# Performance work log

Measured on AMD Instinct MI355X. Metric: run time of the kernel, lower is better.

Reference implementation:

```python
import jax, jax.numpy as jnp
import numpy as np

HEAD_NUM = 16
KEY_DIM = 64
EMBED = 1024
KV_OUT = HEAD_NUM * KEY_DIM  # 1024


def setup_inputs() -> dict:
    key = jax.random.key(0)
    ks = jax.random.split(key, 11)
    B, L, E = 2, 2048, EMBED
    scale = 0.02
    return {
        "query": jax.random.normal(ks[0], (B, L, E), jnp.float32),
        "key": jax.random.normal(ks[1], (B, L, E), jnp.float32),
        "value": jax.random.normal(ks[2], (B, L, E), jnp.float32),
        "W_Query": jax.random.normal(ks[3], (E, KV_OUT), jnp.float32) * scale,
        "W_Key": jax.random.normal(ks[4], (E, KV_OUT), jnp.float32) * scale,
        "W_Value": jax.random.normal(ks[5], (E, KV_OUT), jnp.float32) * scale,
        "W_Output": jax.random.normal(ks[6], (KV_OUT, E), jnp.float32) * scale,
        "B_Query": jnp.zeros((KV_OUT,), jnp.float32),
        "B_Key": jnp.zeros((KV_OUT,), jnp.float32),
        "B_Value": jnp.zeros((KV_OUT,), jnp.float32),
        "B_Output": jnp.zeros((E,), jnp.float32),
    }


def reference(query, key, value, W_Query, W_Key, W_Value, W_Output,
              B_Query, B_Key, B_Value, B_Output):
    B, Lq, E = query.shape
    Lk = key.shape[1]
    H, D = HEAD_NUM, KEY_DIM
    # QKV projections + bias
    q = query @ W_Query + B_Query            # [B, Lq, H*D]
    k = key @ W_Key + B_Key                  # [B, Lk, H*D]
    v = value @ W_Value + B_Value            # [B, Lk, H*D]
    # tf.split(axis=2) per head == reshape to [B, L, H, D]
    q = q.reshape(B, Lq, H, D)
    k = k.reshape(B, Lk, H, D)
    v = v.reshape(B, Lk, H, D)
    # scaled dot-product attention (no mask, dropout=0)
    scores = jnp.einsum("bqhd,bkhd->bhqk", q, k) / (D ** 0.5)
    probs = jax.nn.softmax(scores, axis=-1)
    out = jnp.einsum("bhqk,bkhd->bqhd", probs, v)  # [B, Lq, H, D]
    out = out.reshape(B, Lq, H * D)
    return out @ W_Output + B_Output
```

## Files before the change

kernel.cpp:

```cpp
#include <hip/hip_runtime.h>

using u16 = unsigned short;
using u32 = unsigned int;

typedef __attribute__((ext_vector_type(8))) short bf16x8;
typedef __attribute__((ext_vector_type(4))) float f32x4;
typedef __attribute__((ext_vector_type(4))) u32 u32x4;
typedef __attribute__((ext_vector_type(2))) u32 u32x2;
typedef __attribute__((ext_vector_type(4))) _Float16 f16x4;

#define MFMA_BF16_K32(a, b, c) __builtin_amdgcn_mfma_f32_16x16x32_bf16((a), (b), (c), 0, 0, 0)
#define MFMA_F16_K16(a, b, c) __builtin_amdgcn_mfma_f32_16x16x16f16((a), (b), (c), 0, 0, 0)

#define QSCALE 0.18033688011112042f

extern "C" __device__ float __ocml_native_exp2_f32(float);

__device__ __forceinline__ u16 f2bf(float f) {
  u32 u = __builtin_bit_cast(u32, f);
  return (u16)((u + 0x7fffu + ((u >> 16) & 1u)) >> 16);
}

__device__ __forceinline__ u32 pk_f16(float a, float b) {
  auto v = __builtin_amdgcn_cvt_pkrtz(a, b);
  return __builtin_bit_cast(u32, v);
}

__device__ __forceinline__ void load_lds16(const void* g, void* l) {
  __builtin_amdgcn_global_load_lds((__attribute__((address_space(1))) void*)g,
                                   (__attribute__((address_space(3))) void*)l,
                                   16, 0, 0);
}

#define W0 asm volatile("s_waitcnt vmcnt(0)" ::: "memory")
#define W3 asm volatile("s_waitcnt vmcnt(3)" ::: "memory")
#define W4 asm volatile("s_waitcnt vmcnt(4)" ::: "memory")
#define W8 asm volatile("s_waitcnt vmcnt(8)" ::: "memory")
#define W12 asm volatile("s_waitcnt vmcnt(12)" ::: "memory")
#define LGKM0 asm volatile("s_waitcnt lgkmcnt(0)" ::: "memory")
#define BARRIER                      \
  do {                               \
    __builtin_amdgcn_s_barrier();    \
    asm volatile("" ::: "memory");   \
  } while (0)

__global__ __launch_bounds__(256) void cvt_all_kernel(
    const float* __restrict__ q, const float* __restrict__ k, const float* __restrict__ v,
    u16* __restrict__ oq, u16* __restrict__ ok, u16* __restrict__ ov,
    const float* __restrict__ w0, const float* __restrict__ w1,
    const float* __restrict__ w2, const float* __restrict__ w3,
    u16* __restrict__ d0, u16* __restrict__ d1,
    u16* __restrict__ d2, u16* __restrict__ d3) {
  const int id = blockIdx.x;
  const int tid = threadIdx.x;
  if (id < 6144) {
    const int z = id >> 11, bx = id & 2047;
    const float* s = z == 0 ? q : z == 1 ? k : v;
    u16* d = z == 0 ? oq : z == 1 ? ok : ov;
    int i = (bx * 256 + tid) * 8;
    f32x4 a = *(const f32x4*)(s + i);
    f32x4 b = *(const f32x4*)(s + i + 4);
    u32x4 o;
    o.x = (u32)f2bf(a.x) | ((u32)f2bf(a.y) << 16);
    o.y = (u32)f2bf(a.z) | ((u32)f2bf(a.w) << 16);
    o.z = (u32)f2bf(b.x) | ((u32)f2bf(b.y) << 16);
    o.w = (u32)f2bf(b.z) | ((u32)f2bf(b.w) << 16);
    *(u32x4*)(d + i) = o;
    return;
  }
  __shared__ float t[64][65];
  const int r0 = id - 6144;
  const int z = r0 >> 8, rr0 = r0 & 255;
  const int bx = rr0 & 15, by = rr0 >> 4;
  const float* src = z == 0 ? w0 : z == 1 ? w1 : z == 2 ? w2 : w3;
  u16* dst = z == 0 ? d0 : z == 1 ? d1 : z == 2 ? d2 : d3;
  const float scale = (z == 0) ? QSCALE : 1.0f;
  const int r = tid >> 4, c4 = (tid & 15) * 4;
#pragma unroll
  for (int i = 0; i < 4; ++i) {
    int row = r + i * 16;
    f32x4 vv = *(const f32x4*)(src + (by * 64 + row) * 1024 + bx * 64 + c4);
    t[row][c4 + 0] = vv.x;
    t[row][c4 + 1] = vv.y;
    t[row][c4 + 2] = vv.z;
    t[row][c4 + 3] = vv.w;
  }
  __syncthreads();
  const int rw = tid >> 2, cc = (tid & 3) * 16;
  alignas(16) u16 tmp[16];
#pragma unroll
  for (int j = 0; j < 16; ++j) tmp[j] = f2bf(t[cc + j][rw] * scale);
  u32x4* outp = (u32x4*)(dst + (bx * 64 + rw) * 1024 + by * 64 + cc);
  outp[0] = *(const u32x4*)&tmp[0];
  outp[1] = *(const u32x4*)&tmp[8];
}

#define QKV_STAGE(BUF, KB)                                                    \
  {                                                                           \
    _Pragma("unroll") for (int t = 0; t < 2; ++t) {                           \
      int c = (wave * 2 + t) * 64 + lane;                                     \
      int row = c >> 2, pc = c & 3, sc = pc ^ ((row >> 1) & 3);               \
      load_lds16(A + (m0 + row) * 1024 + (KB) * 32 + sc * 8,                  \
                 &As[BUF][((wave * 2 + t) * 64) * 8]);                        \
    }                                                                         \
    _Pragma("unroll") for (int t = 0; t < 2; ++t) {                           \
      int c = (wave * 2 + t) * 64 + lane;                                     \
      int row = c >> 2, pc = c & 3, sc = pc ^ ((row >> 1) & 3);               \
      load_lds16(Bt + (n0 + row) * 1024 + (KB) * 32 + sc * 8,                 \
                 &Bs[BUF][((wave * 2 + t) * 64) * 8]);                        \
    }                                                                         \
  }

__global__ __launch_bounds__(256) void gemm_qkv_kernel(
    const u16* __restrict__ x0, const u16* __restrict__ x1, const u16* __restrict__ x2,
    const u16* __restrict__ w0, const u16* __restrict__ w1, const u16* __restrict__ w2,
    const float* __restrict__ b0, const float* __restrict__ b1, const float* __restrict__ b2,
    u16* __restrict__ c0, u16* __restrict__ c1, u16* __restrict__ vt) {
  __shared__ u16 As[2][128 * 32];
  __shared__ u16 Bs[2][128 * 32];
  const int lid = blockIdx.x;
  const int xcd = lid & 7, rr = lid >> 3;
  const int nb = rr & 7, slot = rr >> 3;
  const int g = slot * 8 + xcd;
  const int z = g >> 5, m_idx = g & 31;
  const u16* A = z == 0 ? x0 : z == 1 ? x1 : x2;
  const u16* Bt = z == 0 ? w0 : z == 1 ? w1 : w2;
  const float* bias = z == 0 ? b0 : z == 1 ? b1 : b2;
  const float bscale = z == 0 ? QSCALE : 1.0f;
  const int tid = threadIdx.x;
  const int wave = tid >> 6, lane = tid & 63;
  const int l16 = lane & 15, quad = lane >> 4;
  const int wm = wave >> 1, wn = wave & 1;
  const int m0 = m_idx * 128, n0 = nb * 128;

  f32x4 acc[4][4];
  const f32x4 zf = {0.f, 0.f, 0.f, 0.f};
#pragma unroll
  for (int i = 0; i < 4; ++i)
#pragma unroll
    for (int j = 0; j < 4; ++j) acc[i][j] = zf;

  QKV_STAGE(0, 0);
  QKV_STAGE(1, 1);

  const int chq = (l16 >> 1) & 3;
  for (int kb = 0; kb < 32; ++kb) {
    const int cur = kb & 1;
    if (kb < 31) W4; else W0;
    BARRIER;
    bf16x8 af[4], bfv[4];
#pragma unroll
    for (int mt = 0; mt < 4; ++mt)
      af[mt] = *(const bf16x8*)&As[cur][(wm * 64 + mt * 16 + l16) * 32 + (quad ^ chq) * 8];
#pragma unroll
    for (int nt = 0; nt < 4; ++nt)
      bfv[nt] = *(const bf16x8*)&Bs[cur][(wn * 64 + nt * 16 + l16) * 32 + (quad ^ chq) * 8];
#pragma unroll
    for (int mt = 0; mt < 4; ++mt)
#pragma unroll
      for (int nt = 0; nt < 4; ++nt) acc[mt][nt] = MFMA_BF16_K32(af[mt], bfv[nt], acc[mt][nt]);
    LGKM0;
    BARRIER;
    if (kb + 2 < 32) QKV_STAGE(cur, kb + 2);
  }

  float bv[4];
#pragma unroll
  for (int nt = 0; nt < 4; ++nt) bv[nt] = bias[n0 + wn * 64 + nt * 16 + l16] * bscale;
  if (z != 2) {
    u16* C = z == 0 ? c0 : c1;
#pragma unroll
    for (int mt = 0; mt < 4; ++mt)
#pragma unroll
      for (int nt = 0; nt < 4; ++nt)
#pragma unroll
        for (int r = 0; r < 4; ++r) {
          int row = m0 + wm * 64 + mt * 16 + quad * 4 + r;
          int col = n0 + wn * 64 + nt * 16 + l16;
          C[row * 1024 + col] = f2bf(acc[mt][nt][r] + bv[nt]);
        }
  } else {
#pragma unroll
    for (int mt = 0; mt < 4; ++mt)
#pragma unroll
      for (int nt = 0; nt < 4; ++nt) {
        int kvb = m0 + wm * 64 + mt * 16 + quad * 4;
        int bb = kvb >> 11, kv = kvb & 2047;
        int col = n0 + wn * 64 + nt * 16 + l16;
        int h = col >> 6, dt = (col >> 4) & 3, ld = col & 15;
        int pair = bb * 16 + h;
        int kb2 = kv >> 7, chunk = (kv >> 4) & 7, qd = (kv >> 2) & 3;
        f16x4 hv;
#pragma unroll
        for (int r = 0; r < 4; ++r) hv[r] = (_Float16)(acc[mt][nt][r] + bv[nt]);
        u16* dst = vt + ((((pair * 16 + kb2) * 8 + chunk) * 4 + dt) * 256) + qd * 64 + ld * 4;
        *(f16x4*)dst = hv;
      }
  }
}

#define OUT_STAGE(BUF, KB)                                                    \
  {                                                                           \
    {                                                                         \
      int c = wave * 64 + lane;                                               \
      int row = c >> 2, pc = c & 3, sc = pc ^ ((row >> 1) & 3);               \
      load_lds16(A + (m0 + row) * 1024 + (KB) * 32 + sc * 8,                  \
                 &As[BUF][(wave * 64) * 8]);                                  \
    }                                                                         \
    _Pragma("unroll") for (int t = 0; t < 2; ++t) {                           \
      int c = (wave * 2 + t) * 64 + lane;                                     \
      int row = c >> 2, pc = c & 3, sc = pc ^ ((row >> 1) & 3);               \
      load_lds16(Bt + (n0 + row) * 1024 + (KB) * 32 + sc * 8,                 \
                 &Bs[BUF][((wave * 2 + t) * 64) * 8]);                        \
    }                                                                         \
  }

__global__ __launch_bounds__(256) void gemm_out_kernel(const u16* __restrict__ A,
                                                       const u16* __restrict__ Bt,
                                                       const float* __restrict__ bias,
                                                       float* __restrict__ C) {
  __shared__ u16 As[2][64 * 32];
  __shared__ u16 Bs[2][128 * 32];
  const int lid = blockIdx.x;
  const int xcd = lid & 7, rr = lid >> 3;
  const int nb = rr & 7, slot = rr >> 3;
  const int by = slot * 8 + xcd;
  const int tid = threadIdx.x;
  const int wave = tid >> 6, lane = tid & 63;
  const int l16 = lane & 15, quad = lane >> 4;
  const int m0 = by * 64, n0 = nb * 128;

  f32x4 acc[4][2];
  const f32x4 zf = {0.f, 0.f, 0.f, 0.f};
#pragma unroll
  for (int i = 0; i < 4; ++i)
#pragma unroll
    for (int j = 0; j < 2; ++j) acc[i][j] = zf;

  OUT_STAGE(0, 0);
  OUT_STAGE(1, 1);

  const int chq = (l16 >> 1) & 3;
  for (int kb = 0; kb < 32; ++kb) {
    const int cur = kb & 1;
    if (kb < 31) W3; else W0;
    BARRIER;
    bf16x8 af[4], bfv[2];
#pragma unroll
    for (int mt = 0; mt < 4; ++mt)
      af[mt] = *(const bf16x8*)&As[cur][(mt * 16 + l16) * 32 + (quad ^ chq) * 8];
#pragma unroll
    for (int nt = 0; nt < 2; ++nt)
      bfv[nt] = *(const bf16x8*)&Bs[cur][(wave * 32 + nt * 16 + l16) * 32 + (quad ^ chq) * 8];
#pragma unroll
    for (int mt = 0; mt < 4; ++mt)
#pragma unroll
      for (int nt = 0; nt < 2; ++nt) acc[mt][nt] = MFMA_BF16_K32(af[mt], bfv[nt], acc[mt][nt]);
    LGKM0;
    BARRIER;
    if (kb + 2 < 32) OUT_STAGE(cur, kb + 2);
  }

  float bv[2];
#pragma unroll
  for (int nt = 0; nt < 2; ++nt) bv[nt] = bias[n0 + wave * 32 + nt * 16 + l16];
#pragma unroll
  for (int mt = 0; mt < 4; ++mt)
#pragma unroll
    for (int nt = 0; nt < 2; ++nt)
#pragma unroll
      for (int r = 0; r < 4; ++r) {
        int row = m0 + mt * 16 + quad * 4 + r;
        int col = n0 + wave * 32 + nt * 16 + l16;
        C[row * 1024 + col] = acc[mt][nt][r] + bv[nt];
      }
}

union PU { u32 u[2]; f16x4 v; };

#define QK_EXP(CUR, PKV)                                                          \
  _Pragma("unroll") for (int c2 = 0; c2 < 2; ++c2) {                              \
    const int chunk = wave * 2 + c2;                                              \
    f32x4 s_acc[4];                                                               \
    _Pragma("unroll") for (int qn = 0; qn < 4; ++qn) s_acc[qn] = zf;              \
    _Pragma("unroll") for (int ks = 0; ks < 2; ++ks) {                            \
      bf16x8 kf = *(const bf16x8*)&k_lds[CUR][(chunk * 16 + l16) * 64 +           \
                                              ((ks * 4 + quad) ^ l7) * 8];        \
      _Pragma("unroll") for (int qn = 0; qn < 4; ++qn)                            \
        s_acc[qn] = MFMA_BF16_K32(kf, qf[qn][ks], s_acc[qn]);                     \
    }                                                                             \
    _Pragma("unroll") for (int qn = 0; qn < 4; ++qn) {                            \
      float e0 = __ocml_native_exp2_f32(s_acc[qn].x);                             \
      float e1 = __ocml_native_exp2_f32(s_acc[qn].y);                             \
      float e2 = __ocml_native_exp2_f32(s_acc[qn].z);                             \
      float e3 = __ocml_native_exp2_f32(s_acc[qn].w);                             \
      lp[qn] += (e0 + e1) + (e2 + e3);                                            \
      PKV[c2][qn].u[0] = pk_f16(e0, e1);                                          \
      PKV[c2][qn].u[1] = pk_f16(e2, e3);                                          \
    }                                                                             \
  }

#define FLASH_BODY(KB, CUR, VCUR, VNXT, PFV, PFK, WAIT)                           \
  {                                                                               \
    BARRIER;                                                                      \
    if (PFV) {                                                                    \
      const u16* vp = Vh + ((KB) + 1) * 8192;                                     \
      _Pragma("unroll") for (int c2 = 0; c2 < 2; ++c2)                            \
        _Pragma("unroll") for (int dt = 0; dt < 4; ++dt)                          \
          VNXT[c2][dt] =                                                          \
              *(const f16x4*)(vp + ((wave * 2 + c2) * 4 + dt) * 256 + lane * 4);  \
    }                                                                             \
    PU pkv[2][4];                                                                 \
    QK_EXP(CUR, pkv)                                                              \
    LGKM0;                                                                        \
    BARRIER;                                                                      \
    if (PFK) {                                                                    \
      const int kv0 = ((KB) + 2) * 128;                                           \
      _Pragma("unroll") for (int t = 0; t < 4; ++t) {                             \
        int c = (t * 4 + wave) * 64 + lane;                                       \
        int row = c >> 3, sc8 = (c & 7) ^ (row & 7);                              \
        load_lds16(Kh + (kv0 + row) * 1024 + sc8 * 8,                             \
                   &k_lds[CUR][((t * 4 + wave) * 64) * 8]);                       \
      }                                                                           \
    }                                                                             \
    WAIT;                                                                         \
    _Pragma("unroll") for (int c2 = 0; c2 < 2; ++c2)                              \
      _Pragma("unroll") for (int dt = 0; dt < 4; ++dt)                            \
        _Pragma("unroll") for (int qn = 0; qn < 4; ++qn)                          \
          o_acc[qn][dt] = MFMA_F16_K16(pkv[c2][qn].v, VCUR[c2][dt], o_acc[qn][dt]); \
  }

__global__ __launch_bounds__(256, 2) void flash_kernel(const u16* __restrict__ Q,
                                                       const u16* __restrict__ K,
                                                       const u16* __restrict__ Vt,
                                                       u16* __restrict__ O) {
  __shared__ u16 k_lds[2][128 * 64];
  __shared__ float lred[4][64];
  __shared__ float lfin[64];
  const int tid = threadIdx.x;
  const int wave = tid >> 6, lane = tid & 63;
  const int l16 = lane & 15, quad = lane >> 4;
  const int l7 = l16 & 7;
  const int id = blockIdx.x;
  const int xcd = id & 7, slot = id >> 3;
  const int pair = xcd * 4 + (slot & 3);
  const int qb = slot >> 2;
  const int b = pair >> 4, h = pair & 15;
  const u16* Qh = Q + (b * 2048 + qb * 64) * 1024 + h * 64;
  const u16* Kh = K + b * 2048 * 1024 + h * 64;
  const u16* Vh = Vt + pair * 131072;

#pragma unroll
  for (int t = 0; t < 2; ++t) {
    int c = (t * 4 + wave) * 64 + lane;
    int row = c >> 3, sc8 = (c & 7) ^ (row & 7);
    load_lds16(Qh + row * 1024 + sc8 * 8, &k_lds[0][((t * 4 + wave) * 64) * 8]);
  }
  W0;
  __syncthreads();
  bf16x8 qf[4][2];
#pragma unroll
  for (int qn = 0; qn < 4; ++qn)
#pragma unroll
    for (int ks = 0; ks < 2; ++ks)
      qf[qn][ks] = *(const bf16x8*)&k_lds[0][(qn * 16 + l16) * 64 + (((ks * 4 + quad) ^ l7)) * 8];
  __syncthreads();

#pragma unroll
  for (int t = 0; t < 4; ++t) {
    int c = (t * 4 + wave) * 64 + lane;
    int row = c >> 3, sc8 = (c & 7) ^ (row & 7);
    load_lds16(Kh + row * 1024 + sc8 * 8, &k_lds[0][((t * 4 + wave) * 64) * 8]);
  }
  f16x4 vregA[2][4], vregB[2][4];
#pragma unroll
  for (int c2 = 0; c2 < 2; ++c2)
#pragma unroll
    for (int dt = 0; dt < 4; ++dt)
      vregA[c2][dt] = *(const f16x4*)(Vh + ((wave * 2 + c2) * 4 + dt) * 256 + lane * 4);
#pragma unroll
  for (int t = 0; t < 4; ++t) {
    int c = (t * 4 + wave) * 64 + lane;
    int row = c >> 3, sc8 = (c & 7) ^ (row & 7);
    load_lds16(Kh + (128 + row) * 1024 + sc8 * 8, &k_lds[1][((t * 4 + wave) * 64) * 8]);
  }
  W12;

  f32x4 o_acc[4][4];
  const f32x4 zf = {0.f, 0.f, 0.f, 0.f};
#pragma unroll
  for (int qn = 0; qn < 4; ++qn)
#pragma unroll
    for (int dt = 0; dt < 4; ++dt) o_acc[qn][dt] = zf;
  float lp[4] = {0.f, 0.f, 0.f, 0.f};

  for (int kb2 = 0; kb2 < 7; ++kb2) {
    const int kb = kb2 * 2;
    FLASH_BODY(kb, 0, vregA, vregB, true, true, W12);
    FLASH_BODY(kb + 1, 1, vregB, vregA, true, true, W12);
  }
  FLASH_BODY(14, 0, vregA, vregB, true, false, W8);
  FLASH_BODY(15, 1, vregB, vregA, false, false, W0);

#pragma unroll
  for (int qn = 0; qn < 4; ++qn) {
    lp[qn] += __shfl_xor(lp[qn], 16);
    lp[qn] += __shfl_xor(lp[qn], 32);
  }
  if (quad == 0) {
#pragma unroll
    for (int qn = 0; qn < 4; ++qn) lred[wave][qn * 16 + l16] = lp[qn];
  }
  float* bufA = (float*)&k_lds[0][0];
  float* bufB = (float*)&k_lds[1][0];
  if (wave == 1 || wave == 3) {
    float* buf = (wave == 1) ? bufA : bufB;
#pragma unroll
    for (int qm = 0; qm < 4; ++qm)
#pragma unroll
      for (int dt = 0; dt < 4; ++dt)
        *(f32x4*)&buf[(((qm * 4 + dt) * 4 + quad) * 16 + l16) * 4] = o_acc[qm][dt];
  }
  __syncthreads();
  if (tid < 64) lfin[tid] = lred[0][tid] + lred[1][tid] + lred[2][tid] + lred[3][tid];
  if (wave == 0 || wave == 2) {
    float* buf = (wave == 0) ? bufA : bufB;
#pragma unroll
    for (int qm = 0; qm < 4; ++qm)
#pragma unroll
      for (int dt = 0; dt < 4; ++dt)
        o_acc[qm][dt] += *(const f32x4*)&buf[(((qm * 4 + dt) * 4 + quad) * 16 + l16) * 4];
  }
  __syncthreads();
  if (wave == 2) {
#pragma unroll
    for (int qm = 0; qm < 4; ++qm)
#pragma unroll
      for (int dt = 0; dt < 4; ++dt)
        *(f32x4*)&bufA[(((qm * 4 + dt) * 4 + quad) * 16 + l16) * 4] = o_acc[qm][dt];
  }
  __syncthreads();
  if (wave == 0) {
#pragma unroll
    for (int qm = 0; qm < 4; ++qm)
#pragma unroll
      for (int dt = 0; dt < 4; ++dt)
        o_acc[qm][dt] += *(const f32x4*)&bufA[(((qm * 4 + dt) * 4 + quad) * 16 + l16) * 4];
#pragma unroll
    for (int qm = 0; qm < 4; ++qm)
#pragma unroll
      for (int r = 0; r < 4; ++r) {
        int qrow = qm * 16 + quad * 4 + r;
        float inv = 1.0f / lfin[qrow];
        int row = b * 2048 + qb * 64 + qrow;
#pragma unroll
        for (int dt = 0; dt < 4; ++dt)
          O[row * 1024 + h * 64 + dt * 16 + l16] = f2bf(o_acc[qm][dt][r] * inv);
      }
  }
}

extern "C" void kernel_launch(void* const* d_in, const int* in_sizes, int n_in,
                              void* d_out, int out_size, void* d_ws, size_t ws_size,
                              hipStream_t stream) {
  const float* q = (const float*)d_in[0];
  const float* k = (const float*)d_in[1];
  const float* v = (const float*)d_in[2];
  const float* Wq = (const float*)d_in[3];
  const float* Wk = (const float*)d_in[4];
  const float* Wv = (const float*)d_in[5];
  const float* Wo = (const float*)d_in[6];
  const float* Bq = (const float*)d_in[7];
  const float* Bk = (const float*)d_in[8];
  const float* Bv = (const float*)d_in[9];
  const float* Bo = (const float*)d_in[10];
  float* out = (float*)d_out;

  char* w = (char*)d_ws;
  const size_t MB = 1u << 20;
  u16* xq = (u16*)(w + 0 * MB);
  u16* xk = (u16*)(w + 8 * MB);
  u16* xv = (u16*)(w + 16 * MB);
  u16* wqt = (u16*)(w + 24 * MB);
  u16* wkt = (u16*)(w + 26 * MB);
  u16* wvt = (u16*)(w + 28 * MB);
  u16* wot = (u16*)(w + 30 * MB);
  u16* Qp = (u16*)(w + 32 * MB);
  u16* Kp = (u16*)(w + 40 * MB);
  u16* Vtr = (u16*)(w + 48 * MB);
  u16* At = (u16*)(w + 56 * MB);

  cvt_all_kernel<<<dim3(7168), 256, 0, stream>>>(q, k, v, xq, xk, xv,
                                                 Wq, Wk, Wv, Wo, wqt, wkt, wvt, wot);
  gemm_qkv_kernel<<<dim3(768), 256, 0, stream>>>(xq, xk, xv, wqt, wkt, wvt,
                                                 Bq, Bk, Bv, Qp, Kp, Vtr);
  flash_kernel<<<dim3(1024), 256, 0, stream>>>(Qp, Kp, Vtr, At);
  gemm_out_kernel<<<dim3(512), 256, 0, stream>>>(At, wot, Bo, out);
}
```

Measured before the change: 218.0 us.

## Use 16x16x32 f16 MFMA for PV with repacked V layout and lane-shuffled P

The PV product switches from the K16 f16 MFMA to the K32 f16 MFMA, halving the number of MFMA issues per block. The V projection epilogue writes V^T in a new interleaved layout so each lane loads one 16-byte f16x8 per dt instead of two 8-byte loads, and the wait counts are adjusted for the fewer loads. The P operand is assembled by combining the two kv chunks with cross-lane shuffles (xor 32), which adds shuffle instructions and depends on the new V layout matching the permuted K ordering.

Result: no change. 218.5 us (+0.2%).

```diff
diff --git a/kernel.cpp b/kernel.cpp
--- a/kernel.cpp
+++ b/kernel.cpp
@@ -8,9 +8,10 @@
 typedef __attribute__((ext_vector_type(4))) u32 u32x4;
 typedef __attribute__((ext_vector_type(2))) u32 u32x2;
 typedef __attribute__((ext_vector_type(4))) _Float16 f16x4;
+typedef __attribute__((ext_vector_type(8))) _Float16 f16x8;
 
 #define MFMA_BF16_K32(a, b, c) __builtin_amdgcn_mfma_f32_16x16x32_bf16((a), (b), (c), 0, 0, 0)
-#define MFMA_F16_K16(a, b, c) __builtin_amdgcn_mfma_f32_16x16x16f16((a), (b), (c), 0, 0, 0)
+#define MFMA_F16_K32(a, b, c) __builtin_amdgcn_mfma_f32_16x16x32_f16((a), (b), (c), 0, 0, 0)
 
 #define QSCALE 0.18033688011112042f
 
@@ -36,7 +37,6 @@
 #define W3 asm volatile("s_waitcnt vmcnt(3)" ::: "memory")
 #define W4 asm volatile("s_waitcnt vmcnt(4)" ::: "memory")
 #define W8 asm volatile("s_waitcnt vmcnt(8)" ::: "memory")
-#define W12 asm volatile("s_waitcnt vmcnt(12)" ::: "memory")
 #define LGKM0 asm volatile("s_waitcnt lgkmcnt(0)" ::: "memory")
 #define BARRIER                      \
   do {                               \
@@ -186,14 +186,16 @@
       for (int nt = 0; nt < 4; ++nt) {
         int kvb = m0 + wm * 64 + mt * 16 + quad * 4;
         int bb = kvb >> 11, kv = kvb & 2047;
+        int kb2 = kv >> 7, w = (kv >> 5) & 3;
+        int t = (mt & 1) ? (quad ^ 2) : quad;
+        int j0 = (mt & 1) ? 4 : 0;
         int col = n0 + wn * 64 + nt * 16 + l16;
         int h = col >> 6, dt = (col >> 4) & 3, ld = col & 15;
         int pair = bb * 16 + h;
-        int kb2 = kv >> 7, chunk = (kv >> 4) & 7, qd = (kv >> 2) & 3;
         f16x4 hv;
 #pragma unroll
         for (int r = 0; r < 4; ++r) hv[r] = (_Float16)(acc[mt][nt][r] + bv[nt]);
-        u16* dst = vt + ((((pair * 16 + kb2) * 8 + chunk) * 4 + dt) * 256) + qd * 64 + ld * 4;
+        u16* dst = vt + ((((pair * 16 + kb2) * 4 + w) * 4 + dt) * 512) + (t * 16 + ld) * 8 + j0;
         *(f16x4*)dst = hv;
       }
   }
@@ -276,9 +278,7 @@
       }
 }
 
-union PU { u32 u[2]; f16x4 v; };
-
-#define QK_EXP(CUR, PKV)                                                          \
+#define QK_EXP(CUR)                                                               \
   _Pragma("unroll") for (int c2 = 0; c2 < 2; ++c2) {                              \
     const int chunk = wave * 2 + c2;                                              \
     f32x4 s_acc[4];                                                               \
@@ -295,8 +295,13 @@
       float e2 = __ocml_native_exp2_f32(s_acc[qn].z);                             \
       float e3 = __ocml_native_exp2_f32(s_acc[qn].w);                             \
       lp[qn] += (e0 + e1) + (e2 + e3);                                            \
-      PKV[c2][qn].u[0] = pk_f16(e0, e1);                                          \
-      PKV[c2][qn].u[1] = pk_f16(e2, e3);                                          \
+      if (c2 == 0) {                                                              \
+        p01[qn] = pk_f16(e0, e1);                                                 \
+        p23[qn] = pk_f16(e2, e3);                                                 \
+      } else {                                                                    \
+        s01[qn] = pk_f16(e0, e1);                                                 \
+        s23[qn] = pk_f16(e2, e3);                                                 \
+      }                                                                           \
     }                                                                             \
   }
 
@@ -305,13 +310,20 @@
     BARRIER;                                                                      \
     if (PFV) {                                                                    \
       const u16* vp = Vh + ((KB) + 1) * 8192;                                     \
-      _Pragma("unroll") for (int c2 = 0; c2 < 2; ++c2)                            \
-        _Pragma("unroll") for (int dt = 0; dt < 4; ++dt)                          \
-          VNXT[c2][dt] =                                                          \
-              *(const f16x4*)(vp + ((wave * 2 + c2) * 4 + dt) * 256 + lane * 4);  \
+      _Pragma("unroll") for (int dt = 0; dt < 4; ++dt)                            \
+        VNXT[dt] = *(const f16x8*)(vp + (wave * 4 + dt) * 512 + lane * 8);        \
     }                                                                             \
-    PU pkv[2][4];                                                                 \
-    QK_EXP(CUR, pkv)                                                              \
+    u32 p01[4], p23[4], s01[4], s23[4];                                           \
+    QK_EXP(CUR)                                                                   \
+    f16x8 paf[4];                                                                 \
+    _Pragma("unroll") for (int qn = 0; qn < 4; ++qn) {                            \
+      u32x4 tv;                                                                   \
+      tv.x = p01[qn];                                                             \
+      tv.y = p23[qn];                                                             \
+      tv.z = (u32)__shfl_xor((int)s01[qn], 32);                                   \
+      tv.w = (u32)__shfl_xor((int)s23[qn], 32);                                   \
+      paf[qn] = __builtin_bit_cast(f16x8, tv);                                    \
+    }                                                                             \
     LGKM0;                                                                        \
     BARRIER;                                                                      \
     if (PFK) {                                                                    \
@@ -324,10 +336,9 @@
       }                                                                           \
     }                                                                             \
     WAIT;                                                                         \
-    _Pragma("unroll") for (int c2 = 0; c2 < 2; ++c2)                              \
-      _Pragma("unroll") for (int dt = 0; dt < 4; ++dt)                            \
-        _Pragma("unroll") for (int qn = 0; qn < 4; ++qn)                          \
-          o_acc[qn][dt] = MFMA_F16_K16(pkv[c2][qn].v, VCUR[c2][dt], o_acc[qn][dt]); \
+    _Pragma("unroll") for (int dt = 0; dt < 4; ++dt)                              \
+      _Pragma("unroll") for (int qn = 0; qn < 4; ++qn)                            \
+        o_acc[qn][dt] = MFMA_F16_K32(paf[qn], VCUR[dt], o_acc[qn][dt]);           \
   }
 
 __global__ __launch_bounds__(256, 2) void flash_kernel(const u16* __restrict__ Q,
@@ -372,19 +383,17 @@
     int row = c >> 3, sc8 = (c & 7) ^ (row & 7);
     load_lds16(Kh + row * 1024 + sc8 * 8, &k_lds[0][((t * 4 + wave) * 64) * 8]);
   }
-  f16x4 vregA[2][4], vregB[2][4];
-#pragma unroll
-  for (int c2 = 0; c2 < 2; ++c2)
-#pragma unroll
-    for (int dt = 0; dt < 4; ++dt)
-      vregA[c2][dt] = *(const f16x4*)(Vh + ((wave * 2 + c2) * 4 + dt) * 256 + lane * 4);
+  f16x8 vregA[4], vregB[4];
+#pragma unroll
+  for (int dt = 0; dt < 4; ++dt)
+    vregA[dt] = *(const f16x8*)(Vh + (wave * 4 + dt) * 512 + lane * 8);
 #pragma unroll
   for (int t = 0; t < 4; ++t) {
     int c = (t * 4 + wave) * 64 + lane;
     int row = c >> 3, sc8 = (c & 7) ^ (row & 7);
     load_lds16(Kh + (128 + row) * 1024 + sc8 * 8, &k_lds[1][((t * 4 + wave) * 64) * 8]);
   }
-  W12;
+  W8;
 
   f32x4 o_acc[4][4];
   const f32x4 zf = {0.f, 0.f, 0.f, 0.f};
@@ -396,10 +405,10 @@
 
   for (int kb2 = 0; kb2 < 7; ++kb2) {
     const int kb = kb2 * 2;
-    FLASH_BODY(kb, 0, vregA, vregB, true, true, W12);
-    FLASH_BODY(kb + 1, 1, vregB, vregA, true, true, W12);
-  }
-  FLASH_BODY(14, 0, vregA, vregB, true, false, W8);
+    FLASH_BODY(kb, 0, vregA, vregB, true, true, W8);
+    FLASH_BODY(kb + 1, 1, vregB, vregA, true, true, W8);
+  }
+  FLASH_BODY(14, 0, vregA, vregB, true, false, W4);
   FLASH_BODY(15, 1, vregB, vregA, false, false, W0);
 
 #pragma unroll
```
